# Performance work log

Measured on AMD Instinct MI355X. Metric: run time of the kernel, lower is better.

Reference implementation:

```python
import jax, jax.numpy as jnp
import numpy as np

N, E = 100000, 3200000
IN, HID, OUT = 512, 256, 64
K, ALPHA = 10, 0.1


def setup_inputs() -> dict:
    key = jax.random.key(0)
    k1, k2, k3, k4, k5, k6 = jax.random.split(key, 6)
    x = jax.random.normal(k1, (N, IN), dtype=jnp.float32)
    edge_index = jax.random.randint(k2, (2, E), 0, N, dtype=jnp.int64)
    s1 = 1.0 / np.sqrt(IN)
    s2 = 1.0 / np.sqrt(HID)
    # nn.Linear default init: U(-1/sqrt(fan_in), 1/sqrt(fan_in))
    W1 = jax.random.uniform(k3, (IN, HID), jnp.float32, -s1, s1)
    b1 = jax.random.uniform(k4, (HID,), jnp.float32, -s1, s1)
    W2 = jax.random.uniform(k5, (HID, OUT), jnp.float32, -s2, s2)
    b2 = jax.random.uniform(k6, (OUT,), jnp.float32, -s2, s2)
    return {"x": x, "edge_index": edge_index, "W1": W1, "b1": b1, "W2": W2, "b2": b2}


def reference(x, edge_index, W1, b1, W2, b2):
    # MLP (dropout is identity in eval mode)
    h = jax.nn.relu(x @ W1 + b1) @ W2 + b2  # [N, OUT]

    # gcn_norm with self-loops (PyG APPNP default, normalize=True)
    loop = jnp.arange(N, dtype=edge_index.dtype)
    src = jnp.concatenate([edge_index[0], loop])  # message sources
    dst = jnp.concatenate([edge_index[1], loop])  # aggregation targets
    deg = jax.ops.segment_sum(jnp.ones_like(dst, dtype=h.dtype), dst, num_segments=N)
    dinv = jnp.where(deg > 0, jax.lax.rsqrt(jnp.maximum(deg, 1.0)), 0.0)
    norm = (dinv[src] * dinv[dst])[:, None]  # [E+N, 1]

    x0 = h
    def step(hk, _):
        agg = jax.ops.segment_sum(norm * hk[src], dst, num_segments=N)
        return (1.0 - ALPHA) * agg + ALPHA * x0, None

    h, _ = jax.lax.scan(step, h, None, length=K)
    return h
```

## Files before the change

kernel.cpp:

```cpp
#include <hip/hip_runtime.h>
#include <hip/hip_bf16.h>

#define IN_F  512
#define HID_F 256
#define OUT_F 64

#define BSHIFT 9
#define BNODES 512
#define NBK_MAX 256
#define EBUF_CAP 18432
#define CURS 16
#define CHUNK 8192

typedef __attribute__((ext_vector_type(8))) short bf16x8;
typedef __attribute__((ext_vector_type(4))) float f32x4;

__device__ inline unsigned short f2bf(float f) {
    unsigned u = __float_as_uint(f);
    u += 0x7FFFu + ((u >> 16) & 1u);
    return (unsigned short)(u >> 16);
}
__device__ inline float bf2f(unsigned short u) {
    return __uint_as_float(((unsigned)u) << 16);
}

__device__ inline bf16x8 cvt8(float4 v0, float4 v1) {
    bf16x8 r;
    r[0] = (short)f2bf(v0.x); r[1] = (short)f2bf(v0.y);
    r[2] = (short)f2bf(v0.z); r[3] = (short)f2bf(v0.w);
    r[4] = (short)f2bf(v1.x); r[5] = (short)f2bf(v1.y);
    r[6] = (short)f2bf(v1.z); r[7] = (short)f2bf(v1.w);
    return r;
}

__device__ inline void gload_lds16(const void* g, void* l) {
    __builtin_amdgcn_global_load_lds(
        (const __attribute__((address_space(1))) void*)g,
        (__attribute__((address_space(3))) void*)l, 16, 0, 0);
}

__global__ void prep_w_kernel(const float* __restrict__ W1,
                              const float* __restrict__ W2,
                              unsigned short* __restrict__ W1T,
                              unsigned short* __restrict__ W2T)
{
    int i = blockIdx.x * 256 + threadIdx.x;
    if (i < IN_F * HID_F) {
        int k = i / HID_F, n = i % HID_F;
        W1T[n * IN_F + k] = f2bf(W1[i]);
    }
    if (i < HID_F * OUT_F) {
        int k = i / OUT_F, n = i % OUT_F;
        W2T[n * HID_F + k] = f2bf(W2[i]);
    }
}

__global__ __launch_bounds__(256) void mlp_kernel(
    const float* __restrict__ x, const unsigned short* __restrict__ W1T,
    const float* __restrict__ b1, const unsigned short* __restrict__ W2T,
    const float* __restrict__ b2, const float* __restrict__ dinv,
    unsigned short* __restrict__ h0bf, unsigned short* __restrict__ g0, int N)
{
    __shared__ uint4 smem4[2048];
    char* smem = (char*)smem4;

    const int t  = threadIdx.x;
    const int w  = t >> 6;
    const int l  = t & 63;
    const int lr = l & 15;
    const int lq = l >> 4;
    const int wr = w & 1;
    const int wc = w >> 1;

    const int row0 = blockIdx.x * 64;

    f32x4 acc[2][8];
    #pragma unroll
    for (int s = 0; s < 2; ++s)
        #pragma unroll
        for (int f = 0; f < 8; ++f) acc[s][f] = (f32x4){0.f, 0.f, 0.f, 0.f};

    const int ar0 = row0 + wr * 32 + lr;
    const int ar1 = ar0 + 16;
    const bool av0 = ar0 < N, av1 = ar1 < N;
    const float* xp0 = x + (size_t)ar0 * IN_F + lq * 8;
    const float* xp1 = x + (size_t)ar1 * IN_F + lq * 8;

    for (int ks = 0; ks < 8; ++ks) {
        if (ks) __syncthreads();
        #pragma unroll
        for (int is = 0; is < 8; ++is) {
            int j  = is * 256 + t;
            int n  = j >> 3;
            int cs = (j & 7) ^ (n & 7);
            const unsigned short* src = W1T + (size_t)n * IN_F + ks * 64 + cs * 8;
            char* dst = smem + is * 4096 + (t >> 6) * 1024;
            gload_lds16(src, dst);
        }
        __syncthreads();

        #pragma unroll
        for (int kh = 0; kh < 2; ++kh) {
            const int kofs = ks * 64 + kh * 32;
            bf16x8 a0, a1;
            if (av0) {
                a0 = cvt8(*(const float4*)(xp0 + kofs),
                          *(const float4*)(xp0 + kofs + 4));
            } else {
                #pragma unroll
                for (int j = 0; j < 8; ++j) a0[j] = 0;
            }
            if (av1) {
                a1 = cvt8(*(const float4*)(xp1 + kofs),
                          *(const float4*)(xp1 + kofs + 4));
            } else {
                #pragma unroll
                for (int j = 0; j < 8; ++j) a1[j] = 0;
            }
            #pragma unroll
            for (int f = 0; f < 8; ++f) {
                int n = wc * 128 + f * 16 + lr;
                unsigned off = (unsigned)(n * 128 + kh * 64 + lq * 16);
                bf16x8 b = *(const bf16x8*)(smem + (off ^ ((unsigned)(n & 7) << 4)));
                acc[0][f] = __builtin_amdgcn_mfma_f32_16x16x32_bf16(a0, b, acc[0][f], 0, 0, 0);
                acc[1][f] = __builtin_amdgcn_mfma_f32_16x16x32_bf16(a1, b, acc[1][f], 0, 0, 0);
            }
        }
    }
    __syncthreads();

    #pragma unroll
    for (int f = 0; f < 8; ++f) {
        int c = wc * 128 + f * 16 + lr;
        float bb = b1[c];
        #pragma unroll
        for (int sub = 0; sub < 2; ++sub) {
            #pragma unroll
            for (int j2 = 0; j2 < 4; ++j2) {
                int r = wr * 32 + sub * 16 + lq * 4 + j2;
                float vv = acc[sub][f][j2] + bb;
                vv = vv > 0.f ? vv : 0.f;
                unsigned off = (unsigned)(r * 512 + c * 2);
                *(unsigned short*)(smem + (off ^ ((unsigned)(r & 7) << 4))) = f2bf(vv);
            }
        }
    }
    __syncthreads();

    f32x4 a2[4];
    #pragma unroll
    for (int m = 0; m < 4; ++m) a2[m] = (f32x4){0.f, 0.f, 0.f, 0.f};

    const unsigned short* w2p = W2T + (size_t)(w * 16 + lr) * HID_F + lq * 8;

    #pragma unroll 2
    for (int ks = 0; ks < 8; ++ks) {
        bf16x8 bfrag = *(const bf16x8*)(w2p + ks * 32);
        #pragma unroll
        for (int m = 0; m < 4; ++m) {
            int r = m * 16 + lr;
            unsigned off = (unsigned)(r * 512 + ks * 64 + lq * 16);
            bf16x8 afrag = *(const bf16x8*)(smem + (off ^ ((unsigned)(r & 7) << 4)));
            a2[m] = __builtin_amdgcn_mfma_f32_16x16x32_bf16(afrag, bfrag, a2[m], 0, 0, 0);
        }
    }

    float bb2 = b2[w * 16 + lr];
    #pragma unroll
    for (int m = 0; m < 4; ++m) {
        #pragma unroll
        for (int j2 = 0; j2 < 4; ++j2) {
            int r = row0 + m * 16 + lq * 4 + j2;
            if (r < N) {
                float v = a2[m][j2] + bb2;
                int c = w * 16 + lr;
                h0bf[(size_t)r * OUT_F + c] = f2bf(v);
                g0[(size_t)r * OUT_F + c]   = f2bf(dinv[r] * v);
            }
        }
    }
}

__global__ __launch_bounds__(256) void binned_scatter_kernel(
    const int* __restrict__ src, const int* __restrict__ dst,
    int* __restrict__ bcur, unsigned* __restrict__ ebuf, int E, int nbk)
{
    __shared__ int hist[NBK_MAX];
    __shared__ int gbase[NBK_MAX];
    __shared__ int lcur[NBK_MAX];

    const int t  = threadIdx.x;
    const int bs = blockIdx.x * CHUNK;
    const int nE = min(CHUNK, E - bs);

    if (t < NBK_MAX) { hist[t] = 0; lcur[t] = 0; }
    __syncthreads();

    for (int j = t; j < nE; j += 256)
        atomicAdd(&hist[dst[bs + j] >> BSHIFT], 1);
    __syncthreads();

    for (int b = t; b < nbk; b += 256)
        gbase[b] = hist[b] ? atomicAdd(&bcur[b * CURS], hist[b]) : 0;
    __syncthreads();

    for (int j = t; j < nE; j += 256) {
        int d = dst[bs + j];
        int s = src[bs + j];
        int b = d >> BSHIFT;
        int r = atomicAdd(&lcur[b], 1);
        unsigned pos = (unsigned)(gbase[b] + r);
        if (pos < EBUF_CAP)
            ebuf[(size_t)b * EBUF_CAP + pos] =
                ((unsigned)(d & (BNODES - 1)) << 17) | (unsigned)s;
    }
}

__global__ __launch_bounds__(1024) void bucket_scan_kernel(
    const int* __restrict__ bcur, int* __restrict__ bbase,
    int* __restrict__ off, int nbk, int N, int E)
{
    __shared__ int sm[1024];
    int t = threadIdx.x;
    int v = 0;
    if (t < nbk) {
        v = bcur[t * CURS];
        if (v > EBUF_CAP) v = EBUF_CAP;
    }
    sm[t] = v;
    __syncthreads();
    for (int ofs = 1; ofs < 1024; ofs <<= 1) {
        int x = (t >= ofs) ? sm[t - ofs] : 0;
        __syncthreads();
        sm[t] += x;
        __syncthreads();
    }
    if (t < nbk) bbase[t] = sm[t] - v;
    if (t == nbk - 1) bbase[nbk] = sm[t];
    if (t == 0) off[N] = E;
}

__global__ __launch_bounds__(256) void bucket_build_kernel(
    const unsigned* __restrict__ ebuf, const int* __restrict__ bbase,
    float* __restrict__ dinv, int* __restrict__ off,
    int* __restrict__ csr, int N)
{
    __shared__ int cnt[BNODES];
    __shared__ int loc[BNODES];
    __shared__ int tsum[256];
    const int b = blockIdx.x;
    const int t = threadIdx.x;
    const int beg = bbase[b];
    const int nE  = bbase[b + 1] - beg;
    const unsigned* eb = ebuf + (size_t)b * EBUF_CAP;

    cnt[t] = 0; cnt[t + 256] = 0;
    __syncthreads();
    for (int j = t; j < nE; j += 256)
        atomicAdd(&cnt[eb[j] >> 17], 1);
    __syncthreads();

    int c0 = cnt[2 * t], c1 = cnt[2 * t + 1];
    tsum[t] = c0 + c1;
    __syncthreads();
    for (int ofs = 1; ofs < 256; ofs <<= 1) {
        int v = (t >= ofs) ? tsum[t - ofs] : 0;
        __syncthreads();
        tsum[t] += v;
        __syncthreads();
    }
    int base = (t == 0) ? 0 : tsum[t - 1];
    loc[2 * t]     = beg + base;
    loc[2 * t + 1] = beg + base + c0;
    __syncthreads();

    for (int u = t; u < BNODES; u += 256) {
        int node = b * BNODES + u;
        if (node < N) {
            dinv[node] = rsqrtf((float)(cnt[u] + 1));
            off[node]  = loc[u];
        }
    }
    __syncthreads();
    for (int j = t; j < nE; j += 256) {
        unsigned u = eb[j];
        int pos = atomicAdd(&loc[u >> 17], 1);
        csr[pos] = (int)(u & 0x1FFFFu);
    }
}

__global__ __launch_bounds__(256) void step_kernel(
    const unsigned short* __restrict__ gin,
    const unsigned short* __restrict__ h0bf,
    unsigned short* __restrict__ gout, float* __restrict__ outf,
    const int* __restrict__ off, const int* __restrict__ csr,
    const float* __restrict__ dinv, int N, int last)
{
    const int t    = threadIdx.x;
    const int wid  = (blockIdx.x * 256 + t) >> 6;
    if (wid >= N) return;
    const int lane = t & 63;
    const int q    = lane >> 4;
    const int fb   = lane & 15;

    const uint2* gin2 = (const uint2*)gin;

    float a0 = 0.f, a1 = 0.f, a2 = 0.f, a3 = 0.f;
    const int beg = __builtin_amdgcn_readfirstlane(off[wid]);
    const int end = __builtin_amdgcn_readfirstlane(off[wid + 1]);

    for (int i = beg; i < end; i += 32) {
        int idx[8];
        #pragma unroll
        for (int jj = 0; jj < 8; ++jj) {
            int e = i + jj * 4 + q;
            idx[jj] = (e < end) ? csr[e] : -1;
        }
        uint2 v[8];
        #pragma unroll
        for (int jj = 0; jj < 8; ++jj) {
            v[jj] = (idx[jj] >= 0) ? gin2[(size_t)idx[jj] * 16 + fb]
                                   : make_uint2(0u, 0u);
        }
        #pragma unroll
        for (int jj = 0; jj < 8; ++jj) {
            a0 += bf2f((unsigned short)(v[jj].x & 0xffff));
            a1 += bf2f((unsigned short)(v[jj].x >> 16));
            a2 += bf2f((unsigned short)(v[jj].y & 0xffff));
            a3 += bf2f((unsigned short)(v[jj].y >> 16));
        }
    }

    a0 += __shfl_xor(a0, 16); a0 += __shfl_xor(a0, 32);
    a1 += __shfl_xor(a1, 16); a1 += __shfl_xor(a1, 32);
    a2 += __shfl_xor(a2, 16); a2 += __shfl_xor(a2, 32);
    a3 += __shfl_xor(a3, 16); a3 += __shfl_xor(a3, 32);

    if (q == 0) {
        uint2 sv = gin2[(size_t)wid * 16 + fb];
        uint2 hv = ((const uint2*)h0bf)[(size_t)wid * 16 + fb];
        float dv = dinv[wid];
        float s0 = a0 + bf2f((unsigned short)(sv.x & 0xffff));
        float s1 = a1 + bf2f((unsigned short)(sv.x >> 16));
        float s2 = a2 + bf2f((unsigned short)(sv.y & 0xffff));
        float s3 = a3 + bf2f((unsigned short)(sv.y >> 16));
        float r0 = 0.9f * dv * s0 + 0.1f * bf2f((unsigned short)(hv.x & 0xffff));
        float r1 = 0.9f * dv * s1 + 0.1f * bf2f((unsigned short)(hv.x >> 16));
        float r2 = 0.9f * dv * s2 + 0.1f * bf2f((unsigned short)(hv.y & 0xffff));
        float r3 = 0.9f * dv * s3 + 0.1f * bf2f((unsigned short)(hv.y >> 16));
        if (last) {
            float4 o = make_float4(r0, r1, r2, r3);
            *(float4*)(outf + (size_t)wid * OUT_F + fb * 4) = o;
        } else {
            uint2 g;
            g.x = (unsigned)f2bf(dv * r0) | ((unsigned)f2bf(dv * r1) << 16);
            g.y = (unsigned)f2bf(dv * r2) | ((unsigned)f2bf(dv * r3) << 16);
            ((uint2*)gout)[(size_t)wid * 16 + fb] = g;
        }
    }
}

extern "C" void kernel_launch(void* const* d_in, const int* in_sizes, int n_in,
                              void* d_out, int out_size, void* d_ws, size_t ws_size,
                              hipStream_t stream)
{
    const float* x  = (const float*)d_in[0];
    const int*   ei = (const int*)d_in[1];
    const float* W1 = (const float*)d_in[2];
    const float* b1 = (const float*)d_in[3];
    const float* W2 = (const float*)d_in[4];
    const float* b2 = (const float*)d_in[5];
    float* out = (float*)d_out;

    const int N = in_sizes[0] / IN_F;
    const int E = in_sizes[1] / 2;
    const int* src = ei;
    const int* dst = ei + E;
    const int nbk = (N + BNODES - 1) >> BSHIFT;

    char* wsp = (char*)d_ws;
    auto alloc = [&](size_t bytes) -> char* {
        char* p = wsp;
        wsp += (bytes + 255) & ~(size_t)255;
        return p;
    };
    int*   off  = (int*)  alloc((size_t)(N + 1) * 4);
    float* dinv = (float*)alloc((size_t)N * 4);
    int*   csr  = (int*)  alloc((size_t)E * 4);
    unsigned* ebuf = (unsigned*)alloc((size_t)nbk * EBUF_CAP * 4);
    int*   bcur  = (int*) alloc((size_t)nbk * CURS * 4);
    int*   bbase = (int*) alloc((size_t)(nbk + 1) * 4);
    unsigned short* h0bf = (unsigned short*)alloc((size_t)N * OUT_F * 2);
    unsigned short* gA   = (unsigned short*)alloc((size_t)N * OUT_F * 2);
    unsigned short* gB   = (unsigned short*)alloc((size_t)N * OUT_F * 2);
    unsigned short* W1T  = (unsigned short*)alloc((size_t)IN_F * HID_F * 2);
    unsigned short* W2T  = (unsigned short*)alloc((size_t)HID_F * OUT_F * 2);

    hipMemsetAsync(bcur, 0, (size_t)nbk * CURS * 4, stream);

    const int gScat = (E + CHUNK - 1) / CHUNK;
    binned_scatter_kernel<<<gScat, 256, 0, stream>>>(src, dst, bcur, ebuf, E, nbk);
    bucket_scan_kernel<<<1, 1024, 0, stream>>>(bcur, bbase, off, nbk, N, E);
    bucket_build_kernel<<<nbk, 256, 0, stream>>>(ebuf, bbase, dinv, off, csr, N);

    prep_w_kernel<<<(IN_F * HID_F + 255) / 256, 256, 0, stream>>>(W1, W2, W1T, W2T);
    mlp_kernel<<<(N + 63) / 64, 256, 0, stream>>>(x, W1T, b1, W2T, b2, dinv,
                                                  h0bf, gA, N);

    const int gS = (N + 3) / 4;
    const unsigned short* gin = gA;
    unsigned short* gout = gB;
    for (int k = 0; k < 10; ++k) {
        int last = (k == 9);
        step_kernel<<<gS, 256, 0, stream>>>(gin, h0bf, gout, out, off, csr,
                                            dinv, N, last);
        const unsigned short* tmp = gin;
        gin = gout;
        gout = (unsigned short*)tmp;
    }
}
```

Measured before the change: 782.8 us.

## Split feature halves across XCD groups in propagation, double-buffer MLP weight tiles

```diff
diff --git a/kernel.cpp b/kernel.cpp
--- a/kernel.cpp
+++ b/kernel.cpp
@@ -14,22 +14,23 @@
 
 typedef __attribute__((ext_vector_type(8))) short bf16x8;
 typedef __attribute__((ext_vector_type(4))) float f32x4;
+typedef __attribute__((ext_vector_type(2))) unsigned int u32x2;
 
 __device__ inline unsigned short f2bf(float f) {
     unsigned u = __float_as_uint(f);
     u += 0x7FFFu + ((u >> 16) & 1u);
     return (unsigned short)(u >> 16);
 }
-__device__ inline float bf2f(unsigned short u) {
-    return __uint_as_float(((unsigned)u) << 16);
-}
-
-__device__ inline bf16x8 cvt8(float4 v0, float4 v1) {
+__device__ inline float bf2f(unsigned v) {
+    return __uint_as_float(v << 16);
+}
+
+__device__ inline bf16x8 cvt8(f32x4 v0, f32x4 v1) {
     bf16x8 r;
-    r[0] = (short)f2bf(v0.x); r[1] = (short)f2bf(v0.y);
-    r[2] = (short)f2bf(v0.z); r[3] = (short)f2bf(v0.w);
-    r[4] = (short)f2bf(v1.x); r[5] = (short)f2bf(v1.y);
-    r[6] = (short)f2bf(v1.z); r[7] = (short)f2bf(v1.w);
+    r[0] = (short)f2bf(v0[0]); r[1] = (short)f2bf(v0[1]);
+    r[2] = (short)f2bf(v0[2]); r[3] = (short)f2bf(v0[3]);
+    r[4] = (short)f2bf(v1[0]); r[5] = (short)f2bf(v1[1]);
+    r[6] = (short)f2bf(v1[2]); r[7] = (short)f2bf(v1[3]);
     return r;
 }
 
@@ -55,13 +56,13 @@
     }
 }
 
-__global__ __launch_bounds__(256) void mlp_kernel(
+__global__ __launch_bounds__(512, 4) void mlp_kernel(
     const float* __restrict__ x, const unsigned short* __restrict__ W1T,
     const float* __restrict__ b1, const unsigned short* __restrict__ W2T,
     const float* __restrict__ b2, const float* __restrict__ dinv,
     unsigned short* __restrict__ h0bf, unsigned short* __restrict__ g0, int N)
 {
-    __shared__ uint4 smem4[2048];
+    __shared__ uint4 smem4[4096];
     char* smem = (char*)smem4;
 
     const int t  = threadIdx.x;
@@ -69,10 +70,10 @@
     const int l  = t & 63;
     const int lr = l & 15;
     const int lq = l >> 4;
-    const int wr = w & 1;
-    const int wc = w >> 1;
-
-    const int row0 = blockIdx.x * 64;
+    const int wr = w & 3;
+    const int wc = w >> 2;
+
+    const int row0 = blockIdx.x * 128;
 
     f32x4 acc[2][8];
     #pragma unroll
@@ -86,96 +87,103 @@
     const float* xp0 = x + (size_t)ar0 * IN_F + lq * 8;
     const float* xp1 = x + (size_t)ar1 * IN_F + lq * 8;
 
-    for (int ks = 0; ks < 8; ++ks) {
-        if (ks) __syncthreads();
-        #pragma unroll
-        for (int is = 0; is < 8; ++is) {
-            int j  = is * 256 + t;
+    auto stage = [&](int ks, int buf) {
+        #pragma unroll
+        for (int is = 0; is < 4; ++is) {
+            int j  = is * 512 + t;
             int n  = j >> 3;
             int cs = (j & 7) ^ (n & 7);
-            const unsigned short* src = W1T + (size_t)n * IN_F + ks * 64 + cs * 8;
-            char* dst = smem + is * 4096 + (t >> 6) * 1024;
-            gload_lds16(src, dst);
-        }
-        __syncthreads();
-
+            const unsigned short* srcp = W1T + (size_t)n * IN_F + ks * 64 + cs * 8;
+            char* dstp = smem + buf * 32768 + is * 8192 + (t >> 6) * 1024;
+            gload_lds16(srcp, dstp);
+        }
+    };
+
+    stage(0, 0);
+    __syncthreads();
+
+    for (int ks = 0; ks < 8; ++ks) {
+        if (ks < 7) stage(ks + 1, (ks + 1) & 1);
+        const char* bb = smem + (ks & 1) * 32768;
         #pragma unroll
         for (int kh = 0; kh < 2; ++kh) {
             const int kofs = ks * 64 + kh * 32;
-            bf16x8 a0, a1;
+            bf16x8 a0v, a1v;
             if (av0) {
-                a0 = cvt8(*(const float4*)(xp0 + kofs),
-                          *(const float4*)(xp0 + kofs + 4));
+                a0v = cvt8(*(const f32x4*)(xp0 + kofs),
+                           *(const f32x4*)(xp0 + kofs + 4));
             } else {
                 #pragma unroll
-                for (int j = 0; j < 8; ++j) a0[j] = 0;
+                for (int j = 0; j < 8; ++j) a0v[j] = 0;
             }
             if (av1) {
-                a1 = cvt8(*(const float4*)(xp1 + kofs),
-                          *(const float4*)(xp1 + kofs + 4));
+                a1v = cvt8(*(const f32x4*)(xp1 + kofs),
+                           *(const f32x4*)(xp1 + kofs + 4));
             } else {
                 #pragma unroll
-                for (int j = 0; j < 8; ++j) a1[j] = 0;
+                for (int j = 0; j < 8; ++j) a1v[j] = 0;
             }
             #pragma unroll
             for (int f = 0; f < 8; ++f) {
                 int n = wc * 128 + f * 16 + lr;
                 unsigned off = (unsigned)(n * 128 + kh * 64 + lq * 16);
-                bf16x8 b = *(const bf16x8*)(smem + (off ^ ((unsigned)(n & 7) << 4)));
-                acc[0][f] = __builtin_amdgcn_mfma_f32_16x16x32_bf16(a0, b, acc[0][f], 0, 0, 0);
-                acc[1][f] = __builtin_amdgcn_mfma_f32_16x16x32_bf16(a1, b, acc[1][f], 0, 0, 0);
+                bf16x8 b = *(const bf16x8*)(bb + (off ^ ((unsigned)(n & 7) << 4)));
+                acc[0][f] = __builtin_amdgcn_mfma_f32_16x16x32_bf16(a0v, b, acc[0][f], 0, 0, 0);
+                acc[1][f] = __builtin_amdgcn_mfma_f32_16x16x32_bf16(a1v, b, acc[1][f], 0, 0, 0);
             }
         }
-    }
-    __syncthreads();
+        __syncthreads();
+    }
 
     #pragma unroll
     for (int f = 0; f < 8; ++f) {
         int c = wc * 128 + f * 16 + lr;
-        float bb = b1[c];
+        float bbv = b1[c];
         #pragma unroll
         for (int sub = 0; sub < 2; ++sub) {
             #pragma unroll
             for (int j2 = 0; j2 < 4; ++j2) {
-                int r = wr * 32 + sub * 16 + lq * 4 + j2;
-                float vv = acc[sub][f][j2] + bb;
+                int rr = wr * 32 + sub * 16 + lq * 4 + j2;
+                float vv = acc[sub][f][j2] + bbv;
                 vv = vv > 0.f ? vv : 0.f;
-                unsigned off = (unsigned)(r * 512 + c * 2);
-                *(unsigned short*)(smem + (off ^ ((unsigned)(r & 7) << 4))) = f2bf(vv);
+                unsigned off = (unsigned)(rr * 512 + c * 2);
+                *(unsigned short*)(smem + (off ^ ((unsigned)(rr & 7) << 4))) = f2bf(vv);
             }
         }
     }
     __syncthreads();
 
+    const int ct = w & 3;
+    const int rh = w >> 2;
     f32x4 a2[4];
     #pragma unroll
     for (int m = 0; m < 4; ++m) a2[m] = (f32x4){0.f, 0.f, 0.f, 0.f};
 
-    const unsigned short* w2p = W2T + (size_t)(w * 16 + lr) * HID_F + lq * 8;
+    const unsigned short* w2p = W2T + (size_t)(ct * 16 + lr) * HID_F + lq * 8;
 
     #pragma unroll 2
     for (int ks = 0; ks < 8; ++ks) {
         bf16x8 bfrag = *(const bf16x8*)(w2p + ks * 32);
         #pragma unroll
         for (int m = 0; m < 4; ++m) {
-            int r = m * 16 + lr;
-            unsigned off = (unsigned)(r * 512 + ks * 64 + lq * 16);
-            bf16x8 afrag = *(const bf16x8*)(smem + (off ^ ((unsigned)(r & 7) << 4)));
+            int rr = rh * 64 + m * 16 + lr;
+            unsigned off = (unsigned)(rr * 512 + ks * 64 + lq * 16);
+            bf16x8 afrag = *(const bf16x8*)(smem + (off ^ ((unsigned)(rr & 7) << 4)));
             a2[m] = __builtin_amdgcn_mfma_f32_16x16x32_bf16(afrag, bfrag, a2[m], 0, 0, 0);
         }
     }
 
-    float bb2 = b2[w * 16 + lr];
+    float bb2 = b2[ct * 16 + lr];
     #pragma unroll
     for (int m = 0; m < 4; ++m) {
         #pragma unroll
         for (int j2 = 0; j2 < 4; ++j2) {
-            int r = row0 + m * 16 + lq * 4 + j2;
-            if (r < N) {
+            int rr = row0 + rh * 64 + m * 16 + lq * 4 + j2;
+            if (rr < N) {
                 float v = a2[m][j2] + bb2;
-                int c = w * 16 + lr;
-                h0bf[(size_t)r * OUT_F + c] = f2bf(v);
-                g0[(size_t)r * OUT_F + c]   = f2bf(dinv[r] * v);
+                int c = ct * 16 + lr;
+                h0bf[(size_t)rr * OUT_F + c] = f2bf(v);
+                g0[(size_t)rr * OUT_F + c]   = f2bf(dinv[rr] * v);
             }
         }
     }
@@ -294,68 +302,73 @@
     const unsigned short* __restrict__ h0bf,
     unsigned short* __restrict__ gout, float* __restrict__ outf,
     const int* __restrict__ off, const int* __restrict__ csr,
-    const float* __restrict__ dinv, int N, int last)
-{
+    const float* __restrict__ dinv, int N, int ngrp, int last)
+{
+    const int bid  = blockIdx.x;
+    const int xcd  = bid & 7;
+    const int half = xcd >> 2;
+    const int grp  = (bid >> 3) * 4 + (xcd & 3);
     const int t    = threadIdx.x;
-    const int wid  = (blockIdx.x * 256 + t) >> 6;
-    if (wid >= N) return;
+    const int wid  = grp * 4 + (t >> 6);
+    if (grp >= ngrp || wid >= N) return;
     const int lane = t & 63;
-    const int q    = lane >> 4;
-    const int fb   = lane & 15;
-
-    const uint2* gin2 = (const uint2*)gin;
+    const int q    = lane >> 3;
+    const int fb   = lane & 7;
+
+    const u32x2* gin2 = (const u32x2*)gin;
+    const size_t hbase = (size_t)wid * 16 + half * 8;
 
     float a0 = 0.f, a1 = 0.f, a2 = 0.f, a3 = 0.f;
     const int beg = __builtin_amdgcn_readfirstlane(off[wid]);
     const int end = __builtin_amdgcn_readfirstlane(off[wid + 1]);
 
     for (int i = beg; i < end; i += 32) {
-        int idx[8];
-        #pragma unroll
-        for (int jj = 0; jj < 8; ++jj) {
-            int e = i + jj * 4 + q;
-            idx[jj] = (e < end) ? csr[e] : -1;
-        }
-        uint2 v[8];
-        #pragma unroll
-        for (int jj = 0; jj < 8; ++jj) {
-            v[jj] = (idx[jj] >= 0) ? gin2[(size_t)idx[jj] * 16 + fb]
-                                   : make_uint2(0u, 0u);
-        }
-        #pragma unroll
-        for (int jj = 0; jj < 8; ++jj) {
-            a0 += bf2f((unsigned short)(v[jj].x & 0xffff));
-            a1 += bf2f((unsigned short)(v[jj].x >> 16));
-            a2 += bf2f((unsigned short)(v[jj].y & 0xffff));
-            a3 += bf2f((unsigned short)(v[jj].y >> 16));
-        }
-    }
-
-    a0 += __shfl_xor(a0, 16); a0 += __shfl_xor(a0, 32);
-    a1 += __shfl_xor(a1, 16); a1 += __shfl_xor(a1, 32);
-    a2 += __shfl_xor(a2, 16); a2 += __shfl_xor(a2, 32);
-    a3 += __shfl_xor(a3, 16); a3 += __shfl_xor(a3, 32);
+        int idx[4];
+        #pragma unroll
+        for (int jj = 0; jj < 4; ++jj) {
+            int e = i + jj * 8 + q;
+            idx[jj] = (e < end) ? __builtin_nontemporal_load(csr + e) : -1;
+        }
+        u32x2 v[4];
+        #pragma unroll
+        for (int jj = 0; jj < 4; ++jj)
+            v[jj] = (idx[jj] >= 0) ? gin2[(size_t)idx[jj] * 16 + half * 8 + fb]
+                                   : (u32x2){0u, 0u};
+        #pragma unroll
+        for (int jj = 0; jj < 4; ++jj) {
+            a0 += bf2f(v[jj][0] & 0xffffu);
+            a1 += bf2f(v[jj][0] >> 16);
+            a2 += bf2f(v[jj][1] & 0xffffu);
+            a3 += bf2f(v[jj][1] >> 16);
+        }
+    }
+
+    a0 += __shfl_xor(a0, 8); a0 += __shfl_xor(a0, 16); a0 += __shfl_xor(a0, 32);
+    a1 += __shfl_xor(a1, 8); a1 += __shfl_xor(a1, 16); a1 += __shfl_xor(a1, 32);
+    a2 += __shfl_xor(a2, 8); a2 += __shfl_xor(a2, 16); a2 += __shfl_xor(a2, 32);
+    a3 += __shfl_xor(a3, 8); a3 += __shfl_xor(a3, 16); a3 += __shfl_xor(a3, 32);
 
     if (q == 0) {
-        uint2 sv = gin2[(size_t)wid * 16 + fb];
-        uint2 hv = ((const uint2*)h0bf)[(size_t)wid * 16 + fb];
+        u32x2 sv = gin2[hbase + fb];
+        u32x2 hv = __builtin_nontemporal_load((const u32x2*)h0bf + hbase + fb);
         float dv = dinv[wid];
-        float s0 = a0 + bf2f((unsigned short)(sv.x & 0xffff));
-        float s1 = a1 + bf2f((unsigned short)(sv.x >> 16));
-        float s2 = a2 + bf2f((unsigned short)(sv.y & 0xffff));
-        float s3 = a3 + bf2f((unsigned short)(sv.y >> 16));
-        float r0 = 0.9f * dv * s0 + 0.1f * bf2f((unsigned short)(hv.x & 0xffff));
-        float r1 = 0.9f * dv * s1 + 0.1f * bf2f((unsigned short)(hv.x >> 16));
-        float r2 = 0.9f * dv * s2 + 0.1f * bf2f((unsigned short)(hv.y & 0xffff));
-        float r3 = 0.9f * dv * s3 + 0.1f * bf2f((unsigned short)(hv.y >> 16));
+        float s0 = a0 + bf2f(sv[0] & 0xffffu);
+        float s1 = a1 + bf2f(sv[0] >> 16);
+        float s2 = a2 + bf2f(sv[1] & 0xffffu);
+        float s3 = a3 + bf2f(sv[1] >> 16);
+        float r0 = 0.9f * dv * s0 + 0.1f * bf2f(hv[0] & 0xffffu);
+        float r1 = 0.9f * dv * s1 + 0.1f * bf2f(hv[0] >> 16);
+        float r2 = 0.9f * dv * s2 + 0.1f * bf2f(hv[1] & 0xffffu);
+        float r3 = 0.9f * dv * s3 + 0.1f * bf2f(hv[1] >> 16);
         if (last) {
-            float4 o = make_float4(r0, r1, r2, r3);
-            *(float4*)(outf + (size_t)wid * OUT_F + fb * 4) = o;
+            f32x4 o = (f32x4){r0, r1, r2, r3};
+            __builtin_nontemporal_store(o,
+                (f32x4*)(outf + (size_t)wid * OUT_F + half * 32 + fb * 4));
         } else {
-            uint2 g;
-            g.x = (unsigned)f2bf(dv * r0) | ((unsigned)f2bf(dv * r1) << 16);
-            g.y = (unsigned)f2bf(dv * r2) | ((unsigned)f2bf(dv * r3) << 16);
-            ((uint2*)gout)[(size_t)wid * 16 + fb] = g;
+            u32x2 g;
+            g[0] = (unsigned)f2bf(dv * r0) | ((unsigned)f2bf(dv * r1) << 16);
+            g[1] = (unsigned)f2bf(dv * r2) | ((unsigned)f2bf(dv * r3) << 16);
+            __builtin_nontemporal_store(g, (u32x2*)gout + hbase + fb);
         }
     }
 }
@@ -404,16 +417,17 @@
     bucket_build_kernel<<<nbk, 256, 0, stream>>>(ebuf, bbase, dinv, off, csr, N);
 
     prep_w_kernel<<<(IN_F * HID_F + 255) / 256, 256, 0, stream>>>(W1, W2, W1T, W2T);
-    mlp_kernel<<<(N + 63) / 64, 256, 0, stream>>>(x, W1T, b1, W2T, b2, dinv,
-                                                  h0bf, gA, N);
-
-    const int gS = (N + 3) / 4;
+    mlp_kernel<<<(N + 127) / 128, 512, 0, stream>>>(x, W1T, b1, W2T, b2, dinv,
+                                                    h0bf, gA, N);
+
+    const int ngrp = (N + 3) / 4;
+    const int gS   = 8 * ((ngrp + 3) / 4);
     const unsigned short* gin = gA;
     unsigned short* gout = gB;
     for (int k = 0; k < 10; ++k) {
         int last = (k == 9);
         step_kernel<<<gS, 256, 0, stream>>>(gin, h0bf, gout, out, off, csr,
-                                            dinv, N, last);
+                                            dinv, N, ngrp, last);
         const unsigned short* tmp = gin;
         gin = gout;
         gout = (unsigned short*)tmp;
```

After: 1.291 ms. 1.65x slower.
